# Optimization experiments

Hardware: AMD Instinct MI355X
Metric: run time of the kernel (lower is better)

The kernel has to match this reference:

```python
import jax, jax.numpy as jnp
from jax import lax
import numpy as np

STRIDE = 1
PADDING = 1
THRESHOLD = 0.25
DECAY = 0.9


def setup_inputs() -> dict:
    key = jax.random.key(0)
    k1, k2 = jax.random.split(key)
    B, Cin, L, T = 16, 32, 1024, 64
    Cout, K = 64, 3
    x = jax.random.uniform(k1, (B, Cin, L, T), dtype=jnp.float32)
    weight = jax.random.normal(k2, (Cout, Cin, K), dtype=jnp.float32) * 0.1
    return {"x": x, "weight": weight}


def reference(x, weight):
    # x: (B, Cin, L, T); weight: (Cout, Cin, K)
    B, Cin, L, T = x.shape
    Cout, _, K = weight.shape
    # Conv1d applied to every timestep at once: fold T into the batch dim.
    xt = jnp.transpose(x, (0, 3, 1, 2)).reshape(B * T, Cin, L)  # (B*T, Cin, L)
    act = lax.conv_general_dilated(
        xt, weight,
        window_strides=(STRIDE,),
        padding=[(PADDING, PADDING)],
        dimension_numbers=("NCH", "OIH", "NCH"),
    )  # (B*T, Cout, OL)
    OL = act.shape[-1]
    act = act.reshape(B, T, Cout, OL).transpose(1, 0, 2, 3)  # (T, B, Cout, OL)

    def step(pot, a):
        # LIF update: integrate, decay, threshold, reset (matches original order).
        pot = (pot + a) * DECAY
        spk = (pot >= THRESHOLD).astype(pot.dtype)
        pot = jnp.where(spk > 0, jnp.zeros_like(pot), pot)
        return pot, spk

    pot0 = jnp.zeros((B, Cout, OL), dtype=x.dtype)
    _, spikes = lax.scan(step, pot0, act)  # spikes: (T, B, Cout, OL)
    return jnp.transpose(spikes, (1, 2, 3, 0))  # (B, Cout, OL, T)
```

## Files before the change

### kernel.cpp

```cpp
#include <hip/hip_runtime.h>

#define BB    16
#define CIN   32
#define LEN   1024
#define TT    64
#define COUT  64
#define KK    3

#define TL       16
#define HALO     (TL + 2)
#define NTHREADS 256
#define CO_PER   4
#define NGRAN    (CIN * HALO * 4)
#define NRND     (NGRAN / 64)
#define SPT      (NRND / 4)


__global__ __launch_bounds__(NTHREADS, 4)
void snn_v4(const float* __restrict__ x, const float* __restrict__ w,
            float* __restrict__ out) {
    __shared__ float4 xs[NGRAN];

    const int tid  = threadIdx.x;
    const int l    = tid & (TL - 1);
    const int g    = tid >> 4;
    const int co0  = g * CO_PER;
    const int lane = tid & 63;
    const int wv   = tid >> 6;
    const int l0   = blockIdx.x * TL;
    const int b    = blockIdx.y;

    const float* xb = x + (size_t)b * CIN * LEN * TT;
    const float* wb = w + co0 * (CIN * KK);

    int goff[SPT], loff[SPT];
    unsigned okb = 0u;
    #pragma unroll
    for (int s = 0; s < SPT; ++s) {
        const int G   = (wv + s * 4) * 64 + lane;
        const int ci  = G / (HALO * 4);
        const int rem = G - ci * (HALO * 4);
        const int row = rem >> 2;
        const int h   = rem & 3;
        const int lg  = l0 - 1 + row;
        const bool ok = (lg >= 0) && (lg < LEN);
        okb |= ok ? (1u << s) : 0u;
        goff[s] = (ci * LEN + (ok ? lg : 0)) * TT + h * 4;
        loff[s] = ci * (HALO * 4) + row * 4 + (h ^ ((row >> 1) & 3));
    }

    float    pot[CO_PER] = {0.f, 0.f, 0.f, 0.f};
    unsigned mlo[CO_PER] = {0u, 0u, 0u, 0u};
    unsigned mhi[CO_PER] = {0u, 0u, 0u, 0u};
    float4   tmp[SPT];

    auto issue_loads = [&](int sc) {
        #pragma unroll
        for (int s = 0; s < SPT; ++s) {
            tmp[s] = make_float4(0.f, 0.f, 0.f, 0.f);
            if (okb & (1u << s))
                tmp[s] = *(const float4*)(xb + goff[s] + sc * 16);
        }
    };

    auto substage = [&](int sub, int sc) {
        float acc[CO_PER][8];
        #pragma unroll
        for (int j = 0; j < CO_PER; ++j)
            #pragma unroll
            for (int i = 0; i < 8; ++i) acc[j][i] = 0.f;

        #pragma unroll
        for (int k = 0; k < KK; ++k) {
            const int rowk = l + k;
            const int sw   = (rowk >> 1) & 3;
            const int sA   = rowk * 4 + ((sub * 2)     ^ sw);
            const int sB   = rowk * 4 + ((sub * 2 + 1) ^ sw);
            #pragma unroll 1
            for (int cic = 0; cic < CIN / 4; ++cic) {
                #pragma unroll
                for (int c4 = 0; c4 < 4; ++c4) {
                    const int ci = cic * 4 + c4;
                    const float4 xa = xs[ci * (HALO * 4) + sA];
                    const float4 xc = xs[ci * (HALO * 4) + sB];
                    #pragma unroll
                    for (int j = 0; j < CO_PER; ++j) {
                        const float wj = wb[j * (CIN * KK) + ci * KK + k];
                        acc[j][0] = fmaf(xa.x, wj, acc[j][0]);
                        acc[j][1] = fmaf(xa.y, wj, acc[j][1]);
                        acc[j][2] = fmaf(xa.z, wj, acc[j][2]);
                        acc[j][3] = fmaf(xa.w, wj, acc[j][3]);
                        acc[j][4] = fmaf(xc.x, wj, acc[j][4]);
                        acc[j][5] = fmaf(xc.y, wj, acc[j][5]);
                        acc[j][6] = fmaf(xc.z, wj, acc[j][6]);
                        acc[j][7] = fmaf(xc.w, wj, acc[j][7]);
                    }
                }
            }
        }

        #pragma unroll
        for (int j = 0; j < CO_PER; ++j) {
            unsigned sb = 0u;
            #pragma unroll
            for (int i = 0; i < 8; ++i) {
                const float s  = pot[j] + acc[j][i];
                const float p  = s * 0.9f;
                const bool  sp = (p >= 0.25f);
                sb |= sp ? (1u << i) : 0u;
                pot[j] = sp ? 0.0f : p;
            }
            const unsigned sh = (unsigned)((sc & 1) * 16 + sub * 8);
            if (sc < 2) mlo[j] |= sb << sh;
            else        mhi[j] |= sb << sh;
        }
    };

    #pragma unroll 1
    for (int sc = 0; sc < 4; ++sc) {
        issue_loads(sc);
        __syncthreads();
        #pragma unroll
        for (int s = 0; s < SPT; ++s) xs[loff[s]] = tmp[s];
        __syncthreads();
        substage(0, sc);
        substage(1, sc);
    }

    float* outb = out + (size_t)b * COUT * LEN * TT;
    #pragma unroll
    for (int j = 0; j < CO_PER; ++j) {
        float* dst = outb + ((size_t)(co0 + j) * LEN + (l0 + l)) * TT;
        #pragma unroll
        for (int tq = 0; tq < 16; ++tq) {
            const unsigned word = (tq < 8) ? mlo[j] : mhi[j];
            const unsigned nib  = word >> ((tq & 7) * 4);
            float4 v;
            v.x = (nib & 1u) ? 1.0f : 0.0f;
            v.y = (nib & 2u) ? 1.0f : 0.0f;
            v.z = (nib & 4u) ? 1.0f : 0.0f;
            v.w = (nib & 8u) ? 1.0f : 0.0f;
            *(float4*)(dst + tq * 4) = v;
        }
    }
}

extern "C" void kernel_launch(void* const* d_in, const int* in_sizes, int n_in,
                              void* d_out, int out_size, void* d_ws, size_t ws_size,
                              hipStream_t stream) {
    const float* x = (const float*)d_in[0];
    const float* w = (const float*)d_in[1];
    float* out = (float*)d_out;
    (void)d_ws; (void)ws_size; (void)in_sizes; (void)n_in; (void)out_size;

    hipLaunchKernelGGL(snn_v4, dim3(LEN / TL, BB), dim3(NTHREADS),
                       0, stream, x, w, out);
}
```

Baseline: 624.4 us.

## Rewrite SNN conv kernel with async LDS double-buffering, repacked weights, shuffle-chained LIF

Replaces the kernel with a 512-thread version. Input tiles are loaded straight into double-buffered LDS with global_load_lds, and each wave uses weights repacked by a separate pre-kernel into 8-output-channel groups. Each thread now computes 8 channels over 4 timesteps, and the membrane potential is passed between timestep sub-groups with cross-lane shuffles. Spike outputs are written per pair of time chunks rather than all at the end. The aim is to overlap global loads with compute, cut register staging and improve weight access, at the cost of an extra launch and a serialized four-phase shuffle chain.

```diff
diff --git a/kernel.cpp b/kernel.cpp
--- a/kernel.cpp
+++ b/kernel.cpp
@@ -9,138 +9,160 @@
 
 #define TL       16
 #define HALO     (TL + 2)
-#define NTHREADS 256
-#define CO_PER   4
+#define NTHREADS 512
 #define NGRAN    (CIN * HALO * 4)
-#define NRND     (NGRAN / 64)
-#define SPT      (NRND / 4)
+#define NROUND   (NGRAN / 64)
 
 
+__device__ float wpk2[COUT * CIN * KK];
+__device__ float zeros_g[64];
+
+__global__ void repack_w(const float* __restrict__ w) {
+    const int i = blockIdx.x * 256 + threadIdx.x;
+    if (i < COUT * CIN * KK) {
+        const int j  = i & 7;
+        const int ci = (i >> 3) & 31;
+        const int gk = i >> 8;
+        const int k  = gk % 3;
+        const int g2 = gk / 3;
+        wpk2[i] = w[((g2 * 8 + j) * CIN + ci) * KK + k];
+    }
+}
+
+#define GLD16(GP, LP) __builtin_amdgcn_global_load_lds(                      \
+    (const __attribute__((address_space(1))) void*)(GP),                     \
+    (__attribute__((address_space(3))) void*)(LP), 16, 0, 0)
+
 __global__ __launch_bounds__(NTHREADS, 4)
-void snn_v4(const float* __restrict__ x, const float* __restrict__ w,
-            float* __restrict__ out) {
-    __shared__ float4 xs[NGRAN];
+void snn_v6(const float* __restrict__ x, float* __restrict__ out) {
+    __shared__ float4 xsg[2][NGRAN];
 
     const int tid  = threadIdx.x;
-    const int l    = tid & (TL - 1);
-    const int g    = tid >> 4;
-    const int co0  = g * CO_PER;
+    const int l    = tid & 15;
+    const int tsub = (tid >> 4) & 3;
     const int lane = tid & 63;
-    const int wv   = tid >> 6;
+    const int wv   = __builtin_amdgcn_readfirstlane(tid >> 6);
     const int l0   = blockIdx.x * TL;
     const int b    = blockIdx.y;
+    const int lo   = l0 + l;
 
-    const float* xb = x + (size_t)b * CIN * LEN * TT;
-    const float* wb = w + co0 * (CIN * KK);
+    const float* xb   = x + (size_t)b * CIN * LEN * TT;
+    float*       outb = out + (size_t)b * COUT * LEN * TT;
+    const float* wgb  = wpk2 + wv * (KK * CIN * 8);
 
-    int goff[SPT], loff[SPT];
-    unsigned okb = 0u;
+    const float* src[5];
     #pragma unroll
-    for (int s = 0; s < SPT; ++s) {
-        const int G   = (wv + s * 4) * 64 + lane;
-        const int ci  = G / (HALO * 4);
-        const int rem = G - ci * (HALO * 4);
-        const int row = rem >> 2;
-        const int h   = rem & 3;
-        const int lg  = l0 - 1 + row;
-        const bool ok = (lg >= 0) && (lg < LEN);
-        okb |= ok ? (1u << s) : 0u;
-        goff[s] = (ci * LEN + (ok ? lg : 0)) * TT + h * 4;
-        loff[s] = ci * (HALO * 4) + row * 4 + (h ^ ((row >> 1) & 3));
+    for (int m = 0; m < 5; ++m) {
+        const float* p = zeros_g;
+        const int r = wv + 8 * m;
+        if (r < NROUND) {
+            const int G   = r * 64 + lane;
+            const int ci  = G / (HALO * 4);
+            const int rem = G - ci * (HALO * 4);
+            const int row = rem >> 2;
+            const int h   = rem & 3;
+            const int lg  = l0 - 1 + row;
+            if (lg >= 0 && lg < LEN)
+                p = xb + ((size_t)ci * LEN + lg) * TT + h * 4;
+        }
+        src[m] = p;
     }
 
-    float    pot[CO_PER] = {0.f, 0.f, 0.f, 0.f};
-    unsigned mlo[CO_PER] = {0u, 0u, 0u, 0u};
-    unsigned mhi[CO_PER] = {0u, 0u, 0u, 0u};
-    float4   tmp[SPT];
-
-    auto issue_loads = [&](int sc) {
+    auto issue = [&](int tc, int buf) {
+        char* lb = (char*)&xsg[buf][0];
         #pragma unroll
-        for (int s = 0; s < SPT; ++s) {
-            tmp[s] = make_float4(0.f, 0.f, 0.f, 0.f);
-            if (okb & (1u << s))
-                tmp[s] = *(const float4*)(xb + goff[s] + sc * 16);
-        }
+        for (int m = 0; m < 4; ++m)
+            GLD16(src[m] + tc * 16, lb + (wv + 8 * m) * 1024);
+        if (wv < 4)
+            GLD16(src[4] + tc * 16, lb + (wv + 32) * 1024);
     };
 
-    auto substage = [&](int sub, int sc) {
-        float acc[CO_PER][8];
+    float pot[8];
+    #pragma unroll
+    for (int j = 0; j < 8; ++j) pot[j] = 0.f;
+    unsigned nibp = 0;
+
+    issue(0, 0);
+
+    #pragma unroll 2
+    for (int tc = 0; tc < 4; ++tc) {
+        const int cur = tc & 1;
+        __syncthreads();
+        if (tc + 1 < 4) issue(tc + 1, cur ^ 1);
+
+        const char* xsv = (const char*)&xsg[cur][0] + tsub * 16;
+
+        float acc[8][4];
         #pragma unroll
-        for (int j = 0; j < CO_PER; ++j)
+        for (int j = 0; j < 8; ++j)
             #pragma unroll
-            for (int i = 0; i < 8; ++i) acc[j][i] = 0.f;
+            for (int i = 0; i < 4; ++i) acc[j][i] = 0.f;
 
         #pragma unroll
         for (int k = 0; k < KK; ++k) {
-            const int rowk = l + k;
-            const int sw   = (rowk >> 1) & 3;
-            const int sA   = rowk * 4 + ((sub * 2)     ^ sw);
-            const int sB   = rowk * 4 + ((sub * 2 + 1) ^ sw);
+            const char*  bk = xsv + (l + k) * 64;
+            const float* wk = wgb + k * (CIN * 8);
             #pragma unroll 1
-            for (int cic = 0; cic < CIN / 4; ++cic) {
+            for (int cic = 0; cic < 4; ++cic) {
                 #pragma unroll
-                for (int c4 = 0; c4 < 4; ++c4) {
-                    const int ci = cic * 4 + c4;
-                    const float4 xa = xs[ci * (HALO * 4) + sA];
-                    const float4 xc = xs[ci * (HALO * 4) + sB];
+                for (int c8 = 0; c8 < 8; ++c8) {
+                    const int ci = cic * 8 + c8;
+                    const float4 xr = *(const float4*)(bk + ci * 1152);
+                    const float* wp = wk + ci * 8;
                     #pragma unroll
-                    for (int j = 0; j < CO_PER; ++j) {
-                        const float wj = wb[j * (CIN * KK) + ci * KK + k];
-                        acc[j][0] = fmaf(xa.x, wj, acc[j][0]);
-                        acc[j][1] = fmaf(xa.y, wj, acc[j][1]);
-                        acc[j][2] = fmaf(xa.z, wj, acc[j][2]);
-                        acc[j][3] = fmaf(xa.w, wj, acc[j][3]);
-                        acc[j][4] = fmaf(xc.x, wj, acc[j][4]);
-                        acc[j][5] = fmaf(xc.y, wj, acc[j][5]);
-                        acc[j][6] = fmaf(xc.z, wj, acc[j][6]);
-                        acc[j][7] = fmaf(xc.w, wj, acc[j][7]);
+                    for (int j = 0; j < 8; ++j) {
+                        const float wj = wp[j];
+                        acc[j][0] = fmaf(xr.x, wj, acc[j][0]);
+                        acc[j][1] = fmaf(xr.y, wj, acc[j][1]);
+                        acc[j][2] = fmaf(xr.z, wj, acc[j][2]);
+                        acc[j][3] = fmaf(xr.w, wj, acc[j][3]);
                     }
                 }
             }
         }
 
+        unsigned nibc = 0;
         #pragma unroll
-        for (int j = 0; j < CO_PER; ++j) {
-            unsigned sb = 0u;
+        for (int ph = 0; ph < 4; ++ph) {
+            const int srcl = (((ph + 3) & 3) << 4) | l;
             #pragma unroll
-            for (int i = 0; i < 8; ++i) {
-                const float s  = pot[j] + acc[j][i];
-                const float p  = s * 0.9f;
-                const bool  sp = (p >= 0.25f);
-                sb |= sp ? (1u << i) : 0u;
-                pot[j] = sp ? 0.0f : p;
+            for (int j = 0; j < 8; ++j) {
+                const float pin = __shfl(pot[j], srcl, 64);
+                if (tsub == ph) {
+                    float pp = pin;
+                    unsigned sb = 0;
+                    #pragma unroll
+                    for (int i = 0; i < 4; ++i) {
+                        const float s  = pp + acc[j][i];
+                        const float p  = s * 0.9f;
+                        const bool  sp = (p >= 0.25f);
+                        sb |= sp ? (1u << i) : 0u;
+                        pp = sp ? 0.f : p;
+                    }
+                    pot[j] = pp;
+                    nibc |= sb << (j * 4);
+                }
             }
-            const unsigned sh = (unsigned)((sc & 1) * 16 + sub * 8);
-            if (sc < 2) mlo[j] |= sb << sh;
-            else        mhi[j] |= sb << sh;
         }
-    };
 
-    #pragma unroll 1
-    for (int sc = 0; sc < 4; ++sc) {
-        issue_loads(sc);
-        __syncthreads();
-        #pragma unroll
-        for (int s = 0; s < SPT; ++s) xs[loff[s]] = tmp[s];
-        __syncthreads();
-        substage(0, sc);
-        substage(1, sc);
-    }
-
-    float* outb = out + (size_t)b * COUT * LEN * TT;
-    #pragma unroll
-    for (int j = 0; j < CO_PER; ++j) {
-        float* dst = outb + ((size_t)(co0 + j) * LEN + (l0 + l)) * TT;
-        #pragma unroll
-        for (int tq = 0; tq < 16; ++tq) {
-            const unsigned word = (tq < 8) ? mlo[j] : mhi[j];
-            const unsigned nib  = word >> ((tq & 7) * 4);
-            float4 v;
-            v.x = (nib & 1u) ? 1.0f : 0.0f;
-            v.y = (nib & 2u) ? 1.0f : 0.0f;
-            v.z = (nib & 4u) ? 1.0f : 0.0f;
-            v.w = (nib & 8u) ? 1.0f : 0.0f;
-            *(float4*)(dst + tq * 4) = v;
+        if (cur) {
+            #pragma unroll
+            for (int j = 0; j < 8; ++j) {
+                float* dst = outb + ((size_t)(wv * 8 + j) * LEN + lo) * TT
+                           + (tc - 1) * 16 + tsub * 4;
+                const unsigned n0 = (nibp >> (j * 4)) & 0xFu;
+                const unsigned n1 = (nibc >> (j * 4)) & 0xFu;
+                *(float4*)dst = make_float4(n0 & 1u ? 1.f : 0.f,
+                                            n0 & 2u ? 1.f : 0.f,
+                                            n0 & 4u ? 1.f : 0.f,
+                                            n0 & 8u ? 1.f : 0.f);
+                *(float4*)(dst + 16) = make_float4(n1 & 1u ? 1.f : 0.f,
+                                                   n1 & 2u ? 1.f : 0.f,
+                                                   n1 & 4u ? 1.f : 0.f,
+                                                   n1 & 8u ? 1.f : 0.f);
+            }
+        } else {
+            nibp = nibc;
         }
     }
 }
@@ -153,6 +175,7 @@
     float* out = (float*)d_out;
     (void)d_ws; (void)ws_size; (void)in_sizes; (void)n_in; (void)out_size;
 
-    hipLaunchKernelGGL(snn_v4, dim3(LEN / TL, BB), dim3(NTHREADS),
-                       0, stream, x, w, out);
+    hipLaunchKernelGGL(repack_w, dim3(24), dim3(256), 0, stream, w);
+    hipLaunchKernelGGL(snn_v6, dim3(LEN / TL, BB), dim3(NTHREADS),
+                       0, stream, x, out);
 }
```

Measured after the change: 721.2 us. 1.15x slower.
